# Performance work log

Hardware: AMD Instinct MI355X
Metric: run time of the kernel (lower is better)

## Reference

```python
import jax, jax.numpy as jnp
import numpy as np
from jax import lax

DN3 = ('NDHWC', 'DHWIO', 'NDHWC')
DN2 = ('NHWC', 'HWIO', 'NHWC')


def conv3d(x, w, b, s):
    return lax.conv_general_dilated(x, w, s, 'VALID', dimension_numbers=DN3) + b


def deconv3d(x, w, b, s):
    # Keras Conv3DTranspose, padding='valid': out = (in-1)*stride + kernel
    return lax.conv_transpose(x, w, s, 'VALID', dimension_numbers=DN3) + b


def conv2d_same(x, w):
    return lax.conv_general_dilated(x, w, (1, 1), 'SAME', dimension_numbers=DN2)


def hard_sigmoid(x):
    # Keras ConvLSTM2D default recurrent_activation
    return jnp.clip(0.2 * x + 0.5, 0.0, 1.0)


def convlstm2d(xseq, wx, wh, b):
    # xseq: (B, T, H, W, Cin); wx: (3,3,Cin,4F); wh: (3,3,F,4F); b: (4F,)
    # Inference mode: dropout / recurrent_dropout are identity.
    B, T, H, W, _ = xseq.shape
    F = wh.shape[2]
    xs = jnp.moveaxis(xseq, 1, 0)  # (T, B, H, W, Cin)
    h0 = jnp.zeros((B, H, W, F), xseq.dtype)
    c0 = jnp.zeros((B, H, W, F), xseq.dtype)

    def step(carry, xt):
        h, c = carry
        z = conv2d_same(xt, wx) + conv2d_same(h, wh) + b
        i, f, g, o = jnp.split(z, 4, axis=-1)  # Keras gate order i,f,c,o
        c = hard_sigmoid(f) * c + hard_sigmoid(i) * jnp.tanh(g)
        h = hard_sigmoid(o) * jnp.tanh(c)
        return (h, c), h

    _, hs = lax.scan(step, (h0, c0), xs)
    return jnp.moveaxis(hs, 0, 1)  # (B, T, H, W, F)


def setup_inputs() -> dict:
    key = jax.random.key(0)
    ks = jax.random.split(key, 18)
    g = lambda k, shape, fan: (jax.random.normal(k, shape, jnp.float32) / np.sqrt(fan)).astype(jnp.float32)
    inp = {
        'x': jax.random.normal(ks[0], (8, 227, 227, 10, 1), jnp.float32),
        # encoder Conv3D
        'c1w': g(ks[1], (11, 11, 1, 1, 128), 11 * 11 * 1), 'c1b': jnp.zeros((128,), jnp.float32),
        'c2w': g(ks[2], (5, 5, 1, 128, 64), 5 * 5 * 128), 'c2b': jnp.zeros((64,), jnp.float32),
        # ConvLSTM2D stack (64 -> 32 -> 64 filters)
        'l1x': g(ks[3], (3, 3, 64, 256), 9 * 64), 'l1h': g(ks[4], (3, 3, 64, 256), 9 * 64), 'l1b': jnp.zeros((256,), jnp.float32),
        'l2x': g(ks[5], (3, 3, 64, 128), 9 * 64), 'l2h': g(ks[6], (3, 3, 32, 128), 9 * 32), 'l2b': jnp.zeros((128,), jnp.float32),
        'l3x': g(ks[7], (3, 3, 32, 256), 9 * 32), 'l3h': g(ks[8], (3, 3, 64, 256), 9 * 64), 'l3b': jnp.zeros((256,), jnp.float32),
        # decoder Conv3DTranspose
        'd1w': g(ks[9], (5, 5, 1, 64, 128), 5 * 5 * 64), 'd1b': jnp.zeros((128,), jnp.float32),
        'd2w': g(ks[10], (11, 11, 1, 128, 1), 11 * 11 * 128), 'd2b': jnp.zeros((1,), jnp.float32),
    }
    return inp


def reference(x, c1w, c1b, c2w, c2b, l1x, l1h, l1b, l2x, l2h, l2b,
              l3x, l3h, l3b, d1w, d1b, d2w, d2b):
    e = jax.nn.relu(conv3d(x, c1w, c1b, (4, 4, 1)))   # (B,55,55,10,128)
    e = jax.nn.relu(conv3d(e, c2w, c2b, (2, 2, 1)))   # (B,26,26,10,64)
    # encoded tensor fed straight into ConvLSTM2D: time=26, rows=26, cols=10
    h = convlstm2d(e, l1x, l1h, l1b)                  # (B,26,26,10,64)
    h = convlstm2d(h, l2x, l2h, l2b)                  # (B,26,26,10,32)
    h = convlstm2d(h, l3x, l3h, l3b)                  # (B,26,26,10,64)
    d = jax.nn.relu(deconv3d(h, d1w, d1b, (2, 2, 1)))  # (B,55,55,10,128)
    d = jax.nn.relu(deconv3d(d, d2w, d2b, (4, 4, 1)))  # (B,227,227,10,1)
    return d
```

## Files before the change

### kernel.cpp

```cpp
#include <hip/hip_runtime.h>
#include <math.h>


__device__ __forceinline__ float hsig(float x) {
    float y = 0.2f * x + 0.5f;
    return fminf(fmaxf(y, 0.f), 1.f);
}

__global__ __launch_bounds__(256) void k_conv1(const float* __restrict__ x,
                                               const float* __restrict__ w1,
                                               const float* __restrict__ b1,
                                               float* __restrict__ e1) {
    int bid = blockIdx.x;
    int ht = bid & 3; int tmp = bid >> 2;
    int w = tmp % 10; tmp /= 10;
    int d = tmp % 55; int n = tmp / 55;
    int h0 = ht * 16;

    __shared__ __align__(16) float patch[11][72];
    int tid = threadIdx.x;
    for (int idx = tid; idx < 11 * 71; idx += 256) {
        int j = idx % 71; int kd = idx / 71;
        int rr = d * 4 + kd; int cc = h0 * 4 + j;
        float v = 0.f;
        if (cc < 227) v = x[((n * 227 + rr) * 227 + cc) * 10 + w];
        patch[kd][j] = v;
    }
    __syncthreads();

    int co = tid & 127, pg = tid >> 7;
    float acc[8];
#pragma unroll
    for (int p = 0; p < 8; p++) acc[p] = 0.f;

    for (int kd = 0; kd < 11; kd++) {
        const float4* row = (const float4*)&patch[kd][pg * 32];
        float rr2[40];
#pragma unroll
        for (int q = 0; q < 10; q++) {
            float4 t4 = row[q];
            rr2[4 * q] = t4.x; rr2[4 * q + 1] = t4.y; rr2[4 * q + 2] = t4.z; rr2[4 * q + 3] = t4.w;
        }
        const float* wp = w1 + (kd * 11) * 128 + co;
#pragma unroll
        for (int kh = 0; kh < 11; kh++) {
            float wv = wp[kh * 128];
#pragma unroll
            for (int p = 0; p < 8; p++) acc[p] += rr2[p * 4 + kh] * wv;
        }
    }
    float bv = b1[co];
#pragma unroll
    for (int p = 0; p < 8; p++) {
        int h = h0 + pg * 8 + p;
        if (h < 55)
            e1[(((n * 55 + d) * 55 + h) * 10 + w) * 128 + co] = fmaxf(acc[p] + bv, 0.f);
    }
}

__global__ __launch_bounds__(128) void k_conv2(const float* __restrict__ e1,
                                               const float* __restrict__ w2,
                                               const float* __restrict__ b2,
                                               float* __restrict__ e2) {
    int bid = blockIdx.x;
    int w = bid % 10; int tmp = bid / 10;
    int d = tmp % 26; int n = tmp / 26;

    __shared__ __align__(16) float patch[5][16][60];
    int tid = threadIdx.x;
    int co = tid & 63, pg = tid >> 6;
    float bv = b2[co];
    float acc[14];
#pragma unroll
    for (int p = 0; p < 14; p++) acc[p] = bv;

    for (int c0 = 0; c0 < 128; c0 += 16) {
        __syncthreads();
        for (int idx = tid; idx < 5 * 59 * 16; idx += 128) {
            int ci = idx & 15; int t2 = idx >> 4;
            int col = t2 % 59; int kr = t2 / 59;
            float v = 0.f;
            if (col < 55)
                v = e1[(((n * 55 + d * 2 + kr) * 55 + col) * 10 + w) * 128 + c0 + ci];
            patch[kr][ci][col] = v;
        }
        __syncthreads();
        int base = pg * 28;
        for (int kr = 0; kr < 5; kr++) {
            for (int ci = 0; ci < 16; ci++) {
                const float4* row = (const float4*)&patch[kr][ci][base];
                float rr2[32];
#pragma unroll
                for (int u = 0; u < 8; u++) {
                    float4 t4 = row[u];
                    rr2[4 * u] = t4.x; rr2[4 * u + 1] = t4.y; rr2[4 * u + 2] = t4.z; rr2[4 * u + 3] = t4.w;
                }
                const float* wp = w2 + ((kr * 5) * 128 + c0 + ci) * 64 + co;
#pragma unroll
                for (int kh = 0; kh < 5; kh++) {
                    float wv = wp[kh * 128 * 64];
#pragma unroll
                    for (int p = 0; p < 14; p++) acc[p] += rr2[2 * p + kh] * wv;
                }
            }
        }
    }
#pragma unroll
    for (int p = 0; p < 14; p++) {
        int h = pg * 14 + p;
        if (h < 26)
            e2[(((n * 26 + d) * 26 + h) * 10 + w) * 64 + co] = fmaxf(acc[p], 0.f);
    }
}

template <int CIN, int COUT>
__global__ __launch_bounds__(COUT) void k_xconv(const float* __restrict__ in,
                                                const float* __restrict__ wx,
                                                const float* __restrict__ bias,
                                                float* __restrict__ xz) {
    int bid = blockIdx.x;
    int r = bid % 26; int fr = bid / 26;
    int n = fr / 26, t = fr % 26;

    __shared__ __align__(16) float patch[3][CIN][12];
    int tid = threadIdx.x;
    const float* inf = in + (size_t)fr * (26 * 10 * CIN);
    for (int idx = tid; idx < 3 * 12 * CIN; idx += COUT) {
        int ci = idx % CIN; int t2 = idx / CIN;
        int col = t2 % 12; int kr = t2 / 12;
        int rr = r - 1 + kr; int cc = col - 1;
        float v = 0.f;
        if (rr >= 0 && rr < 26 && cc >= 0 && cc < 10)
            v = inf[(rr * 10 + cc) * CIN + ci];
        patch[kr][ci][col] = v;
    }
    __syncthreads();

    int co = tid;
    float bv = bias[co];
    float acc[10];
#pragma unroll
    for (int c = 0; c < 10; c++) acc[c] = bv;

    for (int kr = 0; kr < 3; kr++) {
        for (int ci0 = 0; ci0 < CIN; ci0 += 4) {
            float wv[4][3];
#pragma unroll
            for (int u = 0; u < 4; u++) {
                const float* wp = wx + ((kr * 3) * CIN + ci0 + u) * COUT + co;
#pragma unroll
                for (int kc = 0; kc < 3; kc++) wv[u][kc] = wp[kc * CIN * COUT];
            }
#pragma unroll
            for (int u = 0; u < 4; u++) {
                const float4* row = (const float4*)&patch[kr][ci0 + u][0];
                float rr2[12];
#pragma unroll
                for (int q = 0; q < 3; q++) {
                    float4 t4 = row[q];
                    rr2[4 * q] = t4.x; rr2[4 * q + 1] = t4.y;
                    rr2[4 * q + 2] = t4.z; rr2[4 * q + 3] = t4.w;
                }
#pragma unroll
                for (int kc = 0; kc < 3; kc++) {
                    float w_ = wv[u][kc];
#pragma unroll
                    for (int c = 0; c < 10; c++) acc[c] += rr2[c + kc] * w_;
                }
            }
        }
    }
    float* outp = xz + ((size_t)(t * 8 + n) * 260 + r * 10) * COUT + co;
#pragma unroll
    for (int c = 0; c < 10; c++) outp[c * COUT] = acc[c];
}

__global__ void k_rst(int* __restrict__ f) {
    if (threadIdx.x < 208)
        __hip_atomic_store(f + threadIdx.x, 0, __ATOMIC_RELAXED,
                           __HIP_MEMORY_SCOPE_AGENT);
}

template <int F, int QS>
__global__ __launch_bounds__(4 * F * QS) void k_lstm(const float* __restrict__ xz,
                                                     const float* __restrict__ wh,
                                                     float* __restrict__ y,
                                                     int* __restrict__ flags) {
    constexpr int C4 = 4 * F;
    constexpr int NT = 4 * F * QS;
    constexpr int CQ = F / QS;
    int bid = blockIdx.x;
    int r = bid % 26; int b = bid / 26;
    int tid = threadIdx.x;
    int co = tid & (C4 - 1);
    int q = tid / C4;
    int ci0 = q * CQ;

    __shared__ __align__(16) float patch[3][F][12];
    __shared__ float zpart[QS][10][C4];

    for (int i = tid; i < 3 * F * 12; i += NT) ((float*)patch)[i] = 0.f;
    __syncthreads();

    float creg = 0.f;
    int gc = tid / F, gf = tid % F;
    int* fl = flags + b * 26;

    for (int t = 0; t < 26; t++) {
        if (t > 0) {
            if (tid < 2) {
                int nb = (tid == 0) ? r - 1 : r + 1;
                if (nb >= 0 && nb < 26) {
                    while (__hip_atomic_load(fl + nb, __ATOMIC_RELAXED,
                                             __HIP_MEMORY_SCOPE_AGENT) < t)
                        __builtin_amdgcn_s_sleep(1);
                }
            }
            __syncthreads();

            for (int i = tid; i < 2 * 10 * F; i += NT) {
                int ci = i % F; int t2 = i / F;
                int col = t2 % 10; int s = t2 / 10;
                int kr = 2 * s; int rr = r - 1 + kr;
                float v = 0.f;
                if (rr >= 0 && rr < 26)
                    v = __hip_atomic_load(
                        &y[((((size_t)b * 26 + (t - 1)) * 26 + rr) * 10 + col) * F + ci],
                        __ATOMIC_RELAXED, __HIP_MEMORY_SCOPE_AGENT);
                patch[kr][ci][col + 1] = v;
            }
            __syncthreads();
        }

        float acc[10];
        if (q == 0) {
            const float* xp = xz + ((size_t)(t * 8 + b) * 260 + r * 10) * C4 + co;
#pragma unroll
            for (int c = 0; c < 10; c++) acc[c] = xp[c * C4];
        } else {
#pragma unroll
            for (int c = 0; c < 10; c++) acc[c] = 0.f;
        }

        if (t > 0) {
            const int krseq[3] = {1, 0, 2};
            for (int kk = 0; kk < 3; kk++) {
                const int kr = krseq[kk];
                for (int cu = 0; cu < CQ; cu += 4) {
                    float wv[4][3];
#pragma unroll
                    for (int u = 0; u < 4; u++) {
                        const float* wp = wh + ((kr * 3) * F + ci0 + cu + u) * C4 + co;
#pragma unroll
                        for (int kc = 0; kc < 3; kc++) wv[u][kc] = wp[kc * F * C4];
                    }
#pragma unroll
                    for (int u = 0; u < 4; u++) {
                        const float4* row = (const float4*)&patch[kr][ci0 + cu + u][0];
                        float rr2[12];
#pragma unroll
                        for (int v4 = 0; v4 < 3; v4++) {
                            float4 t4 = row[v4];
                            rr2[4 * v4] = t4.x; rr2[4 * v4 + 1] = t4.y;
                            rr2[4 * v4 + 2] = t4.z; rr2[4 * v4 + 3] = t4.w;
                        }
#pragma unroll
                        for (int kc = 0; kc < 3; kc++) {
                            float w_ = wv[u][kc];
#pragma unroll
                            for (int c = 0; c < 10; c++) acc[c] += rr2[c + kc] * w_;
                        }
                    }
                }
            }
        }

#pragma unroll
        for (int c = 0; c < 10; c++) zpart[q][c][co] = acc[c];
        __syncthreads();

        if (tid < 10 * F) {
            float zi = 0.f, zf = 0.f, zg = 0.f, zo = 0.f;
#pragma unroll
            for (int qq = 0; qq < QS; qq++) {
                zi += zpart[qq][gc][gf];
                zf += zpart[qq][gc][F + gf];
                zg += zpart[qq][gc][2 * F + gf];
                zo += zpart[qq][gc][3 * F + gf];
            }
            float cn = hsig(zf) * creg + hsig(zi) * tanhf(zg);
            float hn = hsig(zo) * tanhf(cn);
            creg = cn;
            __hip_atomic_store(
                &y[((((size_t)b * 26 + t) * 26 + r) * 10 + gc) * F + gf], hn,
                __ATOMIC_RELAXED, __HIP_MEMORY_SCOPE_AGENT);
            patch[1][gf][gc + 1] = hn;
        }
        __syncthreads();

        if (tid == 0)
            __hip_atomic_store(fl + r, t + 1, __ATOMIC_RELEASE,
                               __HIP_MEMORY_SCOPE_AGENT);
    }
}

__global__ __launch_bounds__(256) void k_deconv1(const float* __restrict__ h3,
                                                 const float* __restrict__ dw,
                                                 const float* __restrict__ db,
                                                 float* __restrict__ out) {
    int bid = blockIdx.x;
    int ht = bid & 1; int tmp = bid >> 1;
    int w = tmp % 10; tmp /= 10;
    int od = tmp % 55; int n = tmp / 55;

    __shared__ __align__(16) float patch[3][64][24];
    int tid = threadIdx.x;
    int odd = od & 1;
    int id0 = odd ? (od - 3) / 2 : od / 2 - 2;
    int ihb = ht * 16 - 2;
    for (int idx = tid; idx < 3 * 20 * 64; idx += 256) {
        int ci = idx & 63; int t2 = idx >> 6;
        int j = t2 % 20; int s = t2 / 20;
        int id = id0 + s; int ih = ihb + j;
        float v = 0.f;
        if (id >= 0 && id < 26 && ih >= 0 && ih < 26)
            v = h3[((((size_t)n * 26 + id) * 26 + ih) * 10 + w) * 64 + ci];
        patch[s][ci][j] = v;
    }
    __syncthreads();

    int co = tid & 127, pg = tid >> 7;
    float acc[16];
#pragma unroll
    for (int p = 0; p < 16; p++) acc[p] = 0.f;

    int nslot = odd ? 2 : 3;
    for (int s = 0; s < nslot; s++) {
        int kd = odd ? (1 + 2 * s) : 2 * s;
        for (int ci = 0; ci < 64; ci++) {
            const float* pr = &patch[s][ci][pg * 8];
            float rr2[10];
            {
                float4 t0 = *(const float4*)pr;
                float4 t1 = *(const float4*)(pr + 4);
                float2 t2v = *(const float2*)(pr + 8);
                rr2[0] = t0.x; rr2[1] = t0.y; rr2[2] = t0.z; rr2[3] = t0.w;
                rr2[4] = t1.x; rr2[5] = t1.y; rr2[6] = t1.z; rr2[7] = t1.w;
                rr2[8] = t2v.x; rr2[9] = t2v.y;
            }
            const float* wp = dw + ((kd * 5) * 64 + ci) * 128 + co;
#pragma unroll
            for (int kh = 0; kh < 5; kh++) {
                float wv = wp[kh * 64 * 128];
                const int po = kh & 1;
                const int rbase = (kh + po) >> 1;
#pragma unroll
                for (int jj = 0; jj < 8; jj++)
                    acc[po + 2 * jj] += rr2[rbase + jj] * wv;
            }
        }
    }
    float bv = db[co];
#pragma unroll
    for (int p = 0; p < 16; p++) {
        int oh = ht * 32 + pg * 16 + p;
        if (oh < 55)
            out[((((size_t)n * 55 + od) * 55 + oh) * 10 + w) * 128 + co] =
                fmaxf(acc[p] + bv, 0.f);
    }
}

__global__ __launch_bounds__(256) void k_dc2_gemm(const float* __restrict__ d1n,
                                                  const float* __restrict__ dw,
                                                  float* __restrict__ Dn) {
    int pix = blockIdx.x * 256 + threadIdx.x;
    bool act = pix < 30250;
    int khalf = blockIdx.y;

    float a[128];
    const float* ap = d1n + (size_t)(act ? pix : 0) * 128;
#pragma unroll
    for (int i = 0; i < 32; i++) {
        float4 v = ((const float4*)ap)[i];
        a[4 * i] = v.x; a[4 * i + 1] = v.y; a[4 * i + 2] = v.z; a[4 * i + 3] = v.w;
    }

    int k0 = khalf * 61;
    int kn = 61 - khalf;
    for (int kk = 0; kk < kn; kk++) {
        int k = k0 + kk;
        const float* wp = dw + k * 128;
        float acc0 = 0.f, acc1 = 0.f, acc2 = 0.f, acc3 = 0.f;
#pragma unroll
        for (int i = 0; i < 32; i++) {
            acc0 += a[4 * i + 0] * wp[4 * i + 0];
            acc1 += a[4 * i + 1] * wp[4 * i + 1];
            acc2 += a[4 * i + 2] * wp[4 * i + 2];
            acc3 += a[4 * i + 3] * wp[4 * i + 3];
        }
        if (act) Dn[k * 30250 + pix] = (acc0 + acc1) + (acc2 + acc3);
    }
}

__global__ __launch_bounds__(256) void k_dc2_scatter(const float* __restrict__ Dn,
                                                     const float* __restrict__ db,
                                                     float* __restrict__ outn) {
    int od = blockIdx.x;
    int pd = od & 3, qd = od >> 2;
    float bv = db[0];

    for (int p = threadIdx.x; p < 2270; p += 256) {
        int w = p % 10, oh = p / 10;
        int ph = oh & 3, qh = oh >> 2;
        float acc = 0.f;
#pragma unroll
        for (int s = 0; s < 3; s++) {
            int kpd = pd + 4 * s; int id = qd - s;
            if (kpd <= 10 && id >= 0 && id < 55) {
                int kd = 10 - kpd;
#pragma unroll
                for (int t = 0; t < 3; t++) {
                    int kph = ph + 4 * t; int ih = qh - t;
                    if (kph <= 10 && ih >= 0 && ih < 55) {
                        int kh = 10 - kph;
                        acc += Dn[(kd * 11 + kh) * 30250 + (id * 55 + ih) * 10 + w];
                    }
                }
            }
        }
        outn[(size_t)od * 2270 + p] = fmaxf(acc + bv, 0.f);
    }
}

extern "C" void kernel_launch(void* const* d_in, const int* in_sizes, int n_in,
                              void* d_out, int out_size, void* d_ws, size_t ws_size,
                              hipStream_t stream) {
    const float* x   = (const float*)d_in[0];
    const float* c1w = (const float*)d_in[1];
    const float* c1b = (const float*)d_in[2];
    const float* c2w = (const float*)d_in[3];
    const float* c2b = (const float*)d_in[4];
    const float* l1x = (const float*)d_in[5];
    const float* l1h = (const float*)d_in[6];
    const float* l1b = (const float*)d_in[7];
    const float* l2x = (const float*)d_in[8];
    const float* l2h = (const float*)d_in[9];
    const float* l2b = (const float*)d_in[10];
    const float* l3x = (const float*)d_in[11];
    const float* l3h = (const float*)d_in[12];
    const float* l3b = (const float*)d_in[13];
    const float* d1w = (const float*)d_in[14];
    const float* d1b = (const float*)d_in[15];
    const float* d2w = (const float*)d_in[16];
    const float* d2b = (const float*)d_in[17];

    float* ws = (float*)d_ws;
    float* A  = ws;
    float* B  = A + 30976000;
    float* C  = B + 3461120;
    float* S  = C + 3461120;
    float* Y1 = A + 20000000;
    float* Y2 = A + 24000000;
    float* Y3 = C;
    float* D  = B;
    int* FL = (int*)S;
    float* OUT = (float*)d_out;

    k_conv1<<<17600, 256, 0, stream>>>(x, c1w, c1b, A);
    k_conv2<<<2080, 128, 0, stream>>>(A, c2w, c2b, B);

    k_xconv<64, 256><<<208 * 26, 256, 0, stream>>>(B, l1x, l1b, A);
    k_rst<<<1, 256, 0, stream>>>(FL);
    k_lstm<64, 4><<<208, 1024, 0, stream>>>(A, l1h, Y1, FL);

    k_xconv<64, 128><<<208 * 26, 128, 0, stream>>>(Y1, l2x, l2b, A);
    k_rst<<<1, 256, 0, stream>>>(FL);
    k_lstm<32, 8><<<208, 1024, 0, stream>>>(A, l2h, Y2, FL);

    k_xconv<32, 256><<<208 * 26, 256, 0, stream>>>(Y2, l3x, l3b, A);
    k_rst<<<1, 256, 0, stream>>>(FL);
    k_lstm<64, 4><<<208, 1024, 0, stream>>>(A, l3h, Y3, FL);

    k_deconv1<<<8800, 256, 0, stream>>>(Y3, d1w, d1b, A);

    for (int n = 0; n < 8; n++) {
        const float* d1n = A + (size_t)n * 3872000;
        float* outn = OUT + (size_t)n * 515290;
        k_dc2_gemm<<<dim3(119, 2), 256, 0, stream>>>(d1n, d2w, D);
        k_dc2_scatter<<<227, 256, 0, stream>>>(D, d2b, outn);
    }
}
```

Measured before the change: 3.828 ms.

## Split conv2 output rows across two blocks with XCD-aware block swizzle

The second encoder convolution now splits each output column of 26 rows into two halves handled by separate blocks. This doubles the grid and shrinks the shared-memory patch to 29 columns per half. Block indices are permuted in groups of 8, which appears aimed at spreading neighbouring work across the GPU's compute dies. Weights are loaded four input channels at a time, before the inner FMA loops, to hide global load latency. The cost is some duplicated halo loads between the two halves and slightly more complex indexing.

```diff
diff --git a/kernel.cpp b/kernel.cpp
--- a/kernel.cpp
+++ b/kernel.cpp
@@ -62,54 +62,72 @@
                                                const float* __restrict__ w2,
                                                const float* __restrict__ b2,
                                                float* __restrict__ e2) {
-    int bid = blockIdx.x;
-    int w = bid % 10; int tmp = bid / 10;
+    int bid = (blockIdx.x & 7) * 520 + (blockIdx.x >> 3);
+    int ht = bid & 1; int tmp = bid >> 1;
+    int w = tmp % 10; tmp /= 10;
     int d = tmp % 26; int n = tmp / 26;
-
-    __shared__ __align__(16) float patch[5][16][60];
+    int cb = ht * 26;
+
+    __shared__ __align__(16) float patch[5][16][32];
     int tid = threadIdx.x;
     int co = tid & 63, pg = tid >> 6;
     float bv = b2[co];
-    float acc[14];
-#pragma unroll
-    for (int p = 0; p < 14; p++) acc[p] = bv;
+    float acc[7];
+#pragma unroll
+    for (int p = 0; p < 7; p++) acc[p] = bv;
+    const int npg = (pg == 0) ? 7 : 6;
 
     for (int c0 = 0; c0 < 128; c0 += 16) {
         __syncthreads();
-        for (int idx = tid; idx < 5 * 59 * 16; idx += 128) {
-            int ci = idx & 15; int t2 = idx >> 4;
-            int col = t2 % 59; int kr = t2 / 59;
+#pragma unroll
+        for (int k = 0; k < 20; k++) {
+            int idx = tid + k * 128;
+            int ci = idx & 15;
+            int col = (idx >> 4) & 31;
+            int kr = idx >> 9;
             float v = 0.f;
-            if (col < 55)
-                v = e1[(((n * 55 + d * 2 + kr) * 55 + col) * 10 + w) * 128 + c0 + ci];
+            if (col < 29)
+                v = e1[(((n * 55 + d * 2 + kr) * 55 + cb + col) * 10 + w) * 128 + c0 + ci];
             patch[kr][ci][col] = v;
         }
         __syncthreads();
-        int base = pg * 28;
+
         for (int kr = 0; kr < 5; kr++) {
-            for (int ci = 0; ci < 16; ci++) {
-                const float4* row = (const float4*)&patch[kr][ci][base];
-                float rr2[32];
-#pragma unroll
-                for (int u = 0; u < 8; u++) {
-                    float4 t4 = row[u];
-                    rr2[4 * u] = t4.x; rr2[4 * u + 1] = t4.y; rr2[4 * u + 2] = t4.z; rr2[4 * u + 3] = t4.w;
-                }
-                const float* wp = w2 + ((kr * 5) * 128 + c0 + ci) * 64 + co;
-#pragma unroll
-                for (int kh = 0; kh < 5; kh++) {
-                    float wv = wp[kh * 128 * 64];
-#pragma unroll
-                    for (int p = 0; p < 14; p++) acc[p] += rr2[2 * p + kh] * wv;
-                }
-            }
-        }
-    }
-#pragma unroll
-    for (int p = 0; p < 14; p++) {
-        int h = pg * 14 + p;
-        if (h < 26)
+            for (int ci0 = 0; ci0 < 16; ci0 += 4) {
+                float wv[4][5];
+#pragma unroll
+                for (int u = 0; u < 4; u++) {
+                    const float* wp = w2 + ((kr * 5) * 128 + c0 + ci0 + u) * 64 + co;
+#pragma unroll
+                    for (int kh = 0; kh < 5; kh++) wv[u][kh] = wp[kh * 128 * 64];
+                }
+#pragma unroll
+                for (int u = 0; u < 4; u++) {
+                    const float4* row = (const float4*)&patch[kr][ci0 + u][pg * 12];
+                    float rr2[20];
+#pragma unroll
+                    for (int q = 0; q < 5; q++) {
+                        float4 t4 = row[q];
+                        rr2[4 * q] = t4.x; rr2[4 * q + 1] = t4.y;
+                        rr2[4 * q + 2] = t4.z; rr2[4 * q + 3] = t4.w;
+                    }
+#pragma unroll
+                    for (int kh = 0; kh < 5; kh++) {
+                        float w_ = wv[u][kh];
+#pragma unroll
+                        for (int p = 0; p < 7; p++)
+                            acc[p] += rr2[2 * p + kh + 2 * pg] * w_;
+                    }
+                }
+            }
+        }
+    }
+#pragma unroll
+    for (int p = 0; p < 7; p++) {
+        if (p < npg) {
+            int h = ht * 13 + pg * 7 + p;
             e2[(((n * 26 + d) * 26 + h) * 10 + w) * 64 + co] = fmaxf(acc[p], 0.f);
+        }
     }
 }
 
@@ -467,7 +485,7 @@
     float* OUT = (float*)d_out;
 
     k_conv1<<<17600, 256, 0, stream>>>(x, c1w, c1b, A);
-    k_conv2<<<2080, 128, 0, stream>>>(A, c2w, c2b, B);
+    k_conv2<<<4160, 128, 0, stream>>>(A, c2w, c2b, B);
 
     k_xconv<64, 256><<<208 * 26, 256, 0, stream>>>(B, l1x, l1b, A);
     k_rst<<<1, 256, 0, stream>>>(FL);
```

New measurement: 7.744 ms. 2.02x slower.
